# Optimization experiments

Hardware: AMD Instinct MI355X
Metric: run time of the kernel (lower is better)

## Reference

```python
import jax, jax.numpy as jnp
import numpy as np

N = 50000    # n_nodes
E = 800000   # n_edges (avg degree 16)
F_IN = 64    # node_features
F_H = 64     # filters


def setup_inputs() -> dict:
    key = jax.random.key(0)
    ks = jax.random.split(key, 24)
    p = lambda k, s: jax.random.normal(k, s, dtype=jnp.float32) * 0.05
    inp = {
        "x": jax.random.normal(ks[0], (N, F_IN), dtype=jnp.float32),
        "edge_index": jax.random.randint(ks[1], (2, E), 0, N, dtype=jnp.int32),
        "edge_weight": jax.random.uniform(ks[2], (E,), dtype=jnp.float32),
    }
    # 6 ChebConvs (K=2): conv_x_z, conv_h_z, conv_x_r, conv_h_r, conv_x_h, conv_h_h
    for i, nm in enumerate(["xz", "hz", "xr", "hr", "xh", "hh"]):
        fin = F_IN if nm[0] == "x" else F_H
        inp[f"W_{nm}0"] = p(ks[3 + 3 * i], (fin, F_H))
        inp[f"W_{nm}1"] = p(ks[4 + 3 * i], (fin, F_H))
        inp[f"b_{nm}"] = p(ks[5 + 3 * i], (F_H,))
    inp["W_lin"] = p(ks[21], (F_H, F_IN))
    inp["b_lin"] = p(ks[22], (F_IN,))
    return inp


def _forward(x, edge_weight, edge_index,
             W_xz0, W_xz1, b_xz, W_hz0, W_hz1, b_hz,
             W_xr0, W_xr1, b_xr, W_hr0, W_hr1, b_hr,
             W_xh0, W_xh1, b_xh, W_hh0, W_hh1, b_hh,
             W_lin, b_lin):
    row, col = edge_index[0], edge_index[1]
    # ChebConv K=2, sym normalization, lambda_max=2: L_hat = -D^{-1/2} A D^{-1/2}
    # (self-loops removed first, as in PyG ChebConv)
    w = jnp.where(row == col, 0.0, edge_weight)
    deg = jax.ops.segment_sum(w, row, num_segments=N)
    deg_safe = jnp.where(deg > 0, deg, 1.0)
    dinv = jnp.where(deg > 0, jax.lax.rsqrt(deg_safe), 0.0)
    norm = -dinv[row] * w * dinv[col]  # [E]

    def conv(v, W0, W1, b):
        # Tx_0 = v ; Tx_1 = L_hat @ v via gather-scatter along edges
        tx1 = jax.ops.segment_sum(norm[:, None] * v[row], col, num_segments=N)
        return v @ W0 + tx1 @ W1 + b

    H = jnp.zeros((N, F_H), dtype=x.dtype)  # initial hidden state
    Z = jax.nn.sigmoid(conv(x, W_xz0, W_xz1, b_xz) + conv(H, W_hz0, W_hz1, b_hz))
    R = jax.nn.sigmoid(conv(x, W_xr0, W_xr1, b_xr) + conv(H, W_hr0, W_hr1, b_hr))
    Ht = jnp.tanh(conv(x, W_xh0, W_xh1, b_xh) + conv(H * R, W_hh0, W_hh1, b_hh))
    H = Z * H + (1.0 - Z) * Ht
    return jax.nn.relu(H) @ W_lin + b_lin


def reference(x, edge_index, edge_weight,
              W_xz0, W_xz1, b_xz, W_hz0, W_hz1, b_hz,
              W_xr0, W_xr1, b_xr, W_hr0, W_hr1, b_hr,
              W_xh0, W_xh1, b_xh, W_hh0, W_hh1, b_hh,
              W_lin, b_lin):
    return _forward(x, edge_weight, edge_index,
                    W_xz0, W_xz1, b_xz, W_hz0, W_hz1, b_hz,
                    W_xr0, W_xr1, b_xr, W_hr0, W_hr1, b_hr,
                    W_xh0, W_xh1, b_xh, W_hh0, W_hh1, b_hh,
                    W_lin, b_lin)
```

## Files before the change

kernel.cpp:

```cpp
#include <hip/hip_runtime.h>

#define N_NODES 50000
#define N_EDGES 800000
#define F 64
#define NPAD 50048
#define NBUCK 196
#define NBLK 256
#define EPB (N_EDGES / NBLK)
#define BN 128
#define ASTRIDE 132

__global__ __launch_bounds__(256) void count_kernel(const int* __restrict__ ei,
                                                    int* __restrict__ cntC,
                                                    int* __restrict__ cntR) {
    __shared__ int histC[NBUCK], histR[NBUCK];
    const int t = threadIdx.x, blk = blockIdx.x;
    for (int i = t; i < NBUCK; i += 256) { histC[i] = 0; histR[i] = 0; }
    __syncthreads();
    const int e0 = blk * EPB;
    for (int i = t; i < EPB; i += 256) {
        int e = e0 + i;
        int r = ei[e], c = ei[N_EDGES + e];
        if (r != c) {
            atomicAdd(&histC[c >> 8], 1);
            atomicAdd(&histR[r >> 8], 1);
        }
    }
    __syncthreads();
    for (int i = t; i < NBUCK; i += 256) {
        cntC[i * NBLK + blk] = histC[i];
        cntR[i * NBLK + blk] = histR[i];
    }
}

__global__ __launch_bounds__(256) void scan1_kernel(int* __restrict__ cntC,
                                                    int* __restrict__ cntR,
                                                    int* __restrict__ btC,
                                                    int* __restrict__ btR) {
    __shared__ int wsum[4];
    const int t = threadIdx.x, g = blockIdx.x;
    int* cnt = (g < NBUCK) ? cntC : cntR;
    int* bt  = (g < NBUCK) ? btC : btR;
    const int bucket = (g < NBUCK) ? g : g - NBUCK;
    const int lane = t & 63, wid = t >> 6;
    int v = cnt[bucket * NBLK + t];
    int s = v;
#pragma unroll
    for (int d = 1; d < 64; d <<= 1) {
        int u = __shfl_up(s, d);
        if (lane >= d) s += u;
    }
    if (lane == 63) wsum[wid] = s;
    __syncthreads();
    int wbase = 0;
    for (int w = 0; w < wid; ++w) wbase += wsum[w];
    cnt[bucket * NBLK + t] = wbase + s - v;
    if (t == 255) bt[bucket] = wbase + s;
}

__global__ __launch_bounds__(256) void scan2_kernel(const int* __restrict__ btC,
                                                    const int* __restrict__ btR,
                                                    int* __restrict__ bbC,
                                                    int* __restrict__ bbR,
                                                    int* __restrict__ offs) {
    __shared__ int wsum[4];
    const int t = threadIdx.x;
    const int lane = t & 63, wid = t >> 6;
    {
        int v = (t < NBUCK) ? btC[t] : 0;
        int s = v;
#pragma unroll
        for (int d = 1; d < 64; d <<= 1) {
            int u = __shfl_up(s, d);
            if (lane >= d) s += u;
        }
        if (lane == 63) wsum[wid] = s;
        __syncthreads();
        int wbase = 0;
        for (int w = 0; w < wid; ++w) wbase += wsum[w];
        if (t < NBUCK) bbC[t] = wbase + s - v;
        if (t == 255) { bbC[NBUCK] = wbase + s; offs[N_NODES] = wbase + s; }
        __syncthreads();
    }
    {
        int v = (t < NBUCK) ? btR[t] : 0;
        int s = v;
#pragma unroll
        for (int d = 1; d < 64; d <<= 1) {
            int u = __shfl_up(s, d);
            if (lane >= d) s += u;
        }
        if (lane == 63) wsum[wid] = s;
        __syncthreads();
        int wbase = 0;
        for (int w = 0; w < wid; ++w) wbase += wsum[w];
        if (t < NBUCK) bbR[t] = wbase + s - v;
        if (t == 255) bbR[NBUCK] = wbase + s;
    }
}

__global__ __launch_bounds__(256) void place_kernel(const int* __restrict__ ei,
                                                    const float* __restrict__ ew,
                                                    const int* __restrict__ cntC,
                                                    const int* __restrict__ cntR,
                                                    const int* __restrict__ bbC,
                                                    const int* __restrict__ bbR,
                                                    uint2* __restrict__ colPart,
                                                    uint2* __restrict__ rowPart) {
    __shared__ int cursC[NBUCK], cursR[NBUCK];
    const int t = threadIdx.x, blk = blockIdx.x;
    for (int i = t; i < NBUCK; i += 256) {
        cursC[i] = bbC[i] + cntC[i * NBLK + blk];
        cursR[i] = bbR[i] + cntR[i * NBLK + blk];
    }
    __syncthreads();
    const int e0 = blk * EPB;
    for (int i = t; i < EPB; i += 256) {
        int e = e0 + i;
        int r = ei[e], c = ei[N_EDGES + e];
        if (r == c) continue;
        unsigned wbits = __float_as_uint(ew[e]);
        int pC = atomicAdd(&cursC[c >> 8], 1);
        colPart[pC] = make_uint2((unsigned)r | ((unsigned)(c & 255) << 16), wbits);
        int pR = atomicAdd(&cursR[r >> 8], 1);
        rowPart[pR] = make_uint2((unsigned)(r & 255), wbits);
    }
}

__global__ __launch_bounds__(256) void rowB_kernel(const uint2* __restrict__ rowPart,
                                                   const int* __restrict__ bbR,
                                                   float* __restrict__ dinv) {
    __shared__ float degL[256];
    const int t = threadIdx.x, b = blockIdx.x;
    degL[t] = 0.0f;
    __syncthreads();
    const int start = bbR[b], end = bbR[b + 1];
    for (int i = start + t; i < end; i += 256) {
        uint2 v = rowPart[i];
        atomicAdd(&degL[v.x], __uint_as_float(v.y));
    }
    __syncthreads();
    int n = b * 256 + t;
    if (n < N_NODES) {
        float d = degL[t];
        dinv[n] = (d > 0.0f) ? rsqrtf(d) : 0.0f;
    }
}

__global__ __launch_bounds__(256) void colB_kernel(const uint2* __restrict__ colPart,
                                                   const int* __restrict__ bbC,
                                                   const float* __restrict__ dinv,
                                                   int* __restrict__ offs,
                                                   uint2* __restrict__ edgesOut) {
    __shared__ int cntL[256];
    __shared__ int curL[256];
    __shared__ int wsum[4];
    const int t = threadIdx.x, b = blockIdx.x;
    const int lane = t & 63, wid = t >> 6;
    const int start = bbC[b], end = bbC[b + 1];
    cntL[t] = 0;
    __syncthreads();
    for (int i = start + t; i < end; i += 256) {
        uint2 v = colPart[i];
        atomicAdd(&cntL[(v.x >> 16) & 255], 1);
    }
    __syncthreads();
    int v = cntL[t];
    int s = v;
#pragma unroll
    for (int d = 1; d < 64; d <<= 1) {
        int u = __shfl_up(s, d);
        if (lane >= d) s += u;
    }
    if (lane == 63) wsum[wid] = s;
    __syncthreads();
    int wbase = 0;
    for (int w = 0; w < wid; ++w) wbase += wsum[w];
    int excl = wbase + s - v;
    curL[t] = excl;
    int n = b * 256 + t;
    if (n < N_NODES) offs[n] = start + excl;
    __syncthreads();
    for (int i = start + t; i < end; i += 256) {
        uint2 e = colPart[i];
        int cl = (e.x >> 16) & 255;
        int p = atomicAdd(&curL[cl], 1);
        int r = e.x & 0xFFFF;
        float wd = __uint_as_float(e.y) * dinv[r];
        edgesOut[start + p] = make_uint2((unsigned)r, __float_as_uint(wd));
    }
}

__global__ __launch_bounds__(256) void gather_kernel(const int* __restrict__ offs,
                                                     const uint2* __restrict__ edgesOut,
                                                     const float* __restrict__ dinv,
                                                     const float* __restrict__ x,
                                                     float* __restrict__ S) {
    int n = blockIdx.x * 4 + (threadIdx.x >> 6);
    int lane = threadIdx.x & 63;
    if (n >= N_NODES) return;
    int p = offs[n], end = offs[n + 1];
    float acc = 0.0f;
    for (int base = p; base < end; base += 32) {
        int rem = end - base;
        int sl = lane & 31;
        uint2 ev = make_uint2(0u, 0u);
        if (sl < rem) ev = edgesOut[base + sl];
        int myr = (int)ev.x;
        float mwd = __uint_as_float(ev.y);
        int cnt = min(rem, 32);
        int i = 0;
        for (; i + 4 <= cnt; i += 4) {
            int r0 = __shfl(myr, i + 0), r1 = __shfl(myr, i + 1);
            int r2 = __shfl(myr, i + 2), r3 = __shfl(myr, i + 3);
            float w0 = __shfl(mwd, i + 0), w1 = __shfl(mwd, i + 1);
            float w2 = __shfl(mwd, i + 2), w3 = __shfl(mwd, i + 3);
            float v0 = x[r0 * F + lane];
            float v1 = x[r1 * F + lane];
            float v2 = x[r2 * F + lane];
            float v3 = x[r3 * F + lane];
            acc = fmaf(w0, v0, acc);
            acc = fmaf(w1, v1, acc);
            acc = fmaf(w2, v2, acc);
            acc = fmaf(w3, v3, acc);
        }
        for (; i < cnt; ++i) {
            int r = __shfl(myr, i);
            float wd = __shfl(mwd, i);
            acc = fmaf(wd, x[r * F + lane], acc);
        }
    }
    S[n * F + lane] = -dinv[n] * acc;
}

__global__ __launch_bounds__(256) void fused_kernel(
    const float* __restrict__ x, float* sOut,
    const float* __restrict__ Wxz0, const float* __restrict__ Wxz1,
    const float* __restrict__ Wxh0, const float* __restrict__ Wxh1,
    const float* __restrict__ bxz, const float* __restrict__ bhz,
    const float* __restrict__ bxh, const float* __restrict__ bhh,
    const float* __restrict__ Wlin, const float* __restrict__ blin) {
    __shared__ float As[64 * ASTRIDE];
    __shared__ float Wc[32 * 128];

    const int t = threadIdx.x;
    const int n0 = blockIdx.x * BN;
    const int ti = t >> 4;
    const int tj = t & 15;
    const int f0 = tj * 4;

    float zacc[8][4], hacc[8][4];
#pragma unroll
    for (int j = 0; j < 4; ++j) {
        float bz = bxz[f0 + j] + bhz[f0 + j];
        float bh = bxh[f0 + j] + bhh[f0 + j];
#pragma unroll
        for (int i = 0; i < 8; ++i) { zacc[i][j] = bz; hacc[i][j] = bh; }
    }

    const int sn = t & 127;
    const int gn_s = n0 + sn;
    const int qb = t >> 7;

    for (int half = 0; half < 2; ++half) {
        const float* Abase = half ? (const float*)sOut : x;
#pragma unroll
        for (int r = 0; r < 8; ++r) {
            int q = r * 2 + qb;
            float4 v = make_float4(0.f, 0.f, 0.f, 0.f);
            if (gn_s < N_NODES) v = *(const float4*)&Abase[gn_s * F + q * 4];
            As[(q * 4 + 0) * ASTRIDE + sn] = v.x;
            As[(q * 4 + 1) * ASTRIDE + sn] = v.y;
            As[(q * 4 + 2) * ASTRIDE + sn] = v.z;
            As[(q * 4 + 3) * ASTRIDE + sn] = v.w;
        }
        const float* Wz = half ? Wxz1 : Wxz0;
        const float* Wh = half ? Wxh1 : Wxh0;
        for (int wchunk = 0; wchunk < 2; ++wchunk) {
            const int kb = wchunk * 32;
#pragma unroll
            for (int r = 0; r < 4; ++r) {
                int idx = r * 256 + t;
                int cq = idx & 31;
                int kk = idx >> 5;
                const float* src = (cq < 16) ? &Wz[(kb + kk) * F + cq * 4]
                                             : &Wh[(kb + kk) * F + (cq - 16) * 4];
                *(float4*)&Wc[kk * 128 + cq * 4] = *(const float4*)src;
            }
            __syncthreads();
#pragma unroll 8
            for (int kk = 0; kk < 32; ++kk) {
                const int kl = kb + kk;
                float4 a0 = *(const float4*)&As[kl * ASTRIDE + ti * 8];
                float4 a1 = *(const float4*)&As[kl * ASTRIDE + ti * 8 + 4];
                float4 wz = *(const float4*)&Wc[kk * 128 + f0];
                float4 wh = *(const float4*)&Wc[kk * 128 + 64 + f0];
                float a[8] = {a0.x, a0.y, a0.z, a0.w, a1.x, a1.y, a1.z, a1.w};
#pragma unroll
                for (int i = 0; i < 8; ++i) {
                    zacc[i][0] = fmaf(a[i], wz.x, zacc[i][0]);
                    zacc[i][1] = fmaf(a[i], wz.y, zacc[i][1]);
                    zacc[i][2] = fmaf(a[i], wz.z, zacc[i][2]);
                    zacc[i][3] = fmaf(a[i], wz.w, zacc[i][3]);
                    hacc[i][0] = fmaf(a[i], wh.x, hacc[i][0]);
                    hacc[i][1] = fmaf(a[i], wh.y, hacc[i][1]);
                    hacc[i][2] = fmaf(a[i], wh.z, hacc[i][2]);
                    hacc[i][3] = fmaf(a[i], wh.w, hacc[i][3]);
                }
            }
            __syncthreads();
        }
    }

#pragma unroll
    for (int j = 0; j < 4; ++j)
#pragma unroll
        for (int i = 0; i < 8; ++i) {
            float zz = 1.0f / (1.0f + __expf(-zacc[i][j]));
            float hh = tanhf(hacc[i][j]);
            float R = fmaxf((1.0f - zz) * hh, 0.0f);
            As[(f0 + j) * ASTRIDE + ti * 8 + i] = R;
        }
#pragma unroll
    for (int r = 0; r < 4; ++r) {
        int idx = r * 256 + t;
        int cq = idx & 15;
        int kk = idx >> 4;
        *(float4*)&Wc[kk * 64 + cq * 4] = *(const float4*)&Wlin[kk * F + cq * 4];
    }
    __syncthreads();

    float oacc[8][4];
#pragma unroll
    for (int j = 0; j < 4; ++j) {
        float bl = blin[f0 + j];
#pragma unroll
        for (int i = 0; i < 8; ++i) oacc[i][j] = bl;
    }
#pragma unroll 8
    for (int k = 0; k < 64; ++k) {
        float4 a0 = *(const float4*)&As[k * ASTRIDE + ti * 8];
        float4 a1 = *(const float4*)&As[k * ASTRIDE + ti * 8 + 4];
        float4 w = *(const float4*)&Wc[k * 64 + f0];
        float a[8] = {a0.x, a0.y, a0.z, a0.w, a1.x, a1.y, a1.z, a1.w};
#pragma unroll
        for (int i = 0; i < 8; ++i) {
            oacc[i][0] = fmaf(a[i], w.x, oacc[i][0]);
            oacc[i][1] = fmaf(a[i], w.y, oacc[i][1]);
            oacc[i][2] = fmaf(a[i], w.z, oacc[i][2]);
            oacc[i][3] = fmaf(a[i], w.w, oacc[i][3]);
        }
    }
#pragma unroll
    for (int i = 0; i < 8; ++i) {
        int gn = n0 + ti * 8 + i;
        if (gn < N_NODES) {
            float4 v = make_float4(oacc[i][0], oacc[i][1], oacc[i][2], oacc[i][3]);
            *(float4*)&sOut[gn * F + f0] = v;
        }
    }
}

__global__ __launch_bounds__(256) void deg_fb(const int* __restrict__ ei,
                                              const float* __restrict__ ew,
                                              float* __restrict__ deg) {
    int e = blockIdx.x * blockDim.x + threadIdx.x;
    if (e >= N_EDGES) return;
    int r = ei[e];
    int c = ei[N_EDGES + e];
    if (r != c) atomicAdd(&deg[r], ew[e]);
}

__global__ __launch_bounds__(256) void dinv_kernel(const float* __restrict__ deg,
                                                   float* __restrict__ dinv) {
    int n = blockIdx.x * blockDim.x + threadIdx.x;
    if (n >= N_NODES) return;
    float d = deg[n];
    dinv[n] = (d > 0.0f) ? rsqrtf(d) : 0.0f;
}

__global__ __launch_bounds__(256) void scatter_fb(const int* __restrict__ ei,
                                                  const float* __restrict__ ew,
                                                  const float* __restrict__ x,
                                                  const float* __restrict__ dinv,
                                                  float* S) {
    int e = blockIdx.x * 4 + (threadIdx.x >> 6);
    int lane = threadIdx.x & 63;
    if (e >= N_EDGES) return;
    int r = ei[e];
    int c = ei[N_EDGES + e];
    if (r == c) return;
    float nrm = -dinv[r] * ew[e] * dinv[c];
    atomicAdd(&S[c * F + lane], nrm * x[r * F + lane]);
}

extern "C" void kernel_launch(void* const* d_in, const int* in_sizes, int n_in,
                              void* d_out, int out_size, void* d_ws, size_t ws_size,
                              hipStream_t stream) {
    const float* x    = (const float*)d_in[0];
    const int*   ei   = (const int*)d_in[1];
    const float* ew   = (const float*)d_in[2];
    const float* Wxz0 = (const float*)d_in[3];
    const float* Wxz1 = (const float*)d_in[4];
    const float* bxz  = (const float*)d_in[5];
    const float* bhz  = (const float*)d_in[8];
    const float* Wxh0 = (const float*)d_in[15];
    const float* Wxh1 = (const float*)d_in[16];
    const float* bxh  = (const float*)d_in[17];
    const float* bhh  = (const float*)d_in[20];
    const float* Wlin = (const float*)d_in[21];
    const float* blin = (const float*)d_in[22];
    float* outp = (float*)d_out;

    int*    cntC  = (int*)d_ws;
    int*    cntR  = cntC + NBUCK * NBLK;
    int*    btC   = cntR + NBUCK * NBLK;
    int*    btR   = btC + 256;
    int*    bbC   = btR + 256;
    int*    bbR   = bbC + 256;
    int*    offs  = bbR + 256;
    float*  dinv  = (float*)(offs + NPAD + 64);
    uint2*  colPart  = (uint2*)(dinv + NPAD);
    uint2*  rowPart  = colPart + N_EDGES;
    uint2*  edgesOut = rowPart + N_EDGES;
    size_t needed = (size_t)(2 * NBUCK * NBLK + 1024 + NPAD + 64 + NPAD) * 4
                  + (size_t)N_EDGES * 3 * 8 + 256;

    if (ws_size >= needed) {
        count_kernel<<<NBLK, 256, 0, stream>>>(ei, cntC, cntR);
        scan1_kernel<<<2 * NBUCK, 256, 0, stream>>>(cntC, cntR, btC, btR);
        scan2_kernel<<<1, 256, 0, stream>>>(btC, btR, bbC, bbR, offs);
        place_kernel<<<NBLK, 256, 0, stream>>>(ei, ew, cntC, cntR, bbC, bbR,
                                               colPart, rowPart);
        rowB_kernel<<<NBUCK, 256, 0, stream>>>(rowPart, bbR, dinv);
        colB_kernel<<<NBUCK, 256, 0, stream>>>(colPart, bbC, dinv, offs, edgesOut);
        gather_kernel<<<(N_NODES + 3) / 4, 256, 0, stream>>>(offs, edgesOut, dinv,
                                                             x, outp);
    } else {
        float* deg = (float*)d_ws;
        float* dv  = deg + NPAD;
        hipMemsetAsync(deg, 0, (size_t)NPAD * sizeof(float), stream);
        hipMemsetAsync(d_out, 0, (size_t)N_NODES * F * sizeof(float), stream);
        deg_fb<<<(N_EDGES + 255) / 256, 256, 0, stream>>>(ei, ew, deg);
        dinv_kernel<<<(N_NODES + 255) / 256, 256, 0, stream>>>(deg, dv);
        scatter_fb<<<N_EDGES / 4, 256, 0, stream>>>(ei, ew, x, dv, outp);
    }
    fused_kernel<<<(N_NODES + BN - 1) / BN, 256, 0, stream>>>(
        x, outp, Wxz0, Wxz1, Wxh0, Wxh1, bxz, bhz, bxh, bhh, Wlin, blin);
}
```

Before: 123.3 us.

## Use 8x8 register tiles with 128 threads and padded LDS layout in fused GEMM

The fused GRU/linear kernel now uses 128 threads per block, with each thread computing an 8-node by 8-feature tile, where it previously computed 8x4. All 64 rows of each weight matrix are staged in LDS in a single pass, and the A tile gains extra padding every 8 rows to reduce bank conflicts. This raises FMA work per LDS load and removes barriers. In exchange it needs about twice the accumulator registers (128 floats) and more LDS, which may lower occupancy and leaves fewer threads per block to hide latency.

```diff
diff --git a/kernel.cpp b/kernel.cpp
--- a/kernel.cpp
+++ b/kernel.cpp
@@ -8,7 +8,7 @@
 #define NBLK 256
 #define EPB (N_EDGES / NBLK)
 #define BN 128
-#define ASTRIDE 132
+#define AIDX(k, n) ((k) * 132 + ((k) >> 3) * 4 + (n))
 
 __global__ __launch_bounds__(256) void count_kernel(const int* __restrict__ ei,
                                                     int* __restrict__ cntC,
@@ -233,130 +233,136 @@
     S[n * F + lane] = -dinv[n] * acc;
 }
 
-__global__ __launch_bounds__(256) void fused_kernel(
+__global__ __launch_bounds__(128) void fused_kernel(
     const float* __restrict__ x, float* sOut,
     const float* __restrict__ Wxz0, const float* __restrict__ Wxz1,
     const float* __restrict__ Wxh0, const float* __restrict__ Wxh1,
     const float* __restrict__ bxz, const float* __restrict__ bhz,
     const float* __restrict__ bxh, const float* __restrict__ bhh,
     const float* __restrict__ Wlin, const float* __restrict__ blin) {
-    __shared__ float As[64 * ASTRIDE];
-    __shared__ float Wc[32 * 128];
+    __shared__ float As[64 * 132 + 32];
+    __shared__ float Wc[64 * 128];
 
     const int t = threadIdx.x;
     const int n0 = blockIdx.x * BN;
-    const int ti = t >> 4;
-    const int tj = t & 15;
-    const int f0 = tj * 4;
-
-    float zacc[8][4], hacc[8][4];
-#pragma unroll
-    for (int j = 0; j < 4; ++j) {
+    const int ti = t >> 3;
+    const int tj = t & 7;
+    const int nb = ti * 8;
+    const int f0 = tj * 8;
+
+    float zacc[8][8], hacc[8][8];
+#pragma unroll
+    for (int j = 0; j < 8; ++j) {
         float bz = bxz[f0 + j] + bhz[f0 + j];
         float bh = bxh[f0 + j] + bhh[f0 + j];
 #pragma unroll
         for (int i = 0; i < 8; ++i) { zacc[i][j] = bz; hacc[i][j] = bh; }
     }
 
-    const int sn = t & 127;
-    const int gn_s = n0 + sn;
-    const int qb = t >> 7;
+    const int gn_s = n0 + t;
 
     for (int half = 0; half < 2; ++half) {
         const float* Abase = half ? (const float*)sOut : x;
 #pragma unroll
-        for (int r = 0; r < 8; ++r) {
-            int q = r * 2 + qb;
+        for (int q = 0; q < 16; ++q) {
             float4 v = make_float4(0.f, 0.f, 0.f, 0.f);
             if (gn_s < N_NODES) v = *(const float4*)&Abase[gn_s * F + q * 4];
-            As[(q * 4 + 0) * ASTRIDE + sn] = v.x;
-            As[(q * 4 + 1) * ASTRIDE + sn] = v.y;
-            As[(q * 4 + 2) * ASTRIDE + sn] = v.z;
-            As[(q * 4 + 3) * ASTRIDE + sn] = v.w;
+            As[AIDX(q * 4 + 0, t)] = v.x;
+            As[AIDX(q * 4 + 1, t)] = v.y;
+            As[AIDX(q * 4 + 2, t)] = v.z;
+            As[AIDX(q * 4 + 3, t)] = v.w;
         }
         const float* Wz = half ? Wxz1 : Wxz0;
         const float* Wh = half ? Wxh1 : Wxh0;
-        for (int wchunk = 0; wchunk < 2; ++wchunk) {
-            const int kb = wchunk * 32;
-#pragma unroll
-            for (int r = 0; r < 4; ++r) {
-                int idx = r * 256 + t;
-                int cq = idx & 31;
-                int kk = idx >> 5;
-                const float* src = (cq < 16) ? &Wz[(kb + kk) * F + cq * 4]
-                                             : &Wh[(kb + kk) * F + (cq - 16) * 4];
-                *(float4*)&Wc[kk * 128 + cq * 4] = *(const float4*)src;
-            }
-            __syncthreads();
+#pragma unroll
+        for (int r = 0; r < 16; ++r) {
+            int idx = r * 128 + t;
+            int cq = idx & 31;
+            int kk = idx >> 5;
+            const float* src = (cq < 16) ? &Wz[kk * F + cq * 4]
+                                         : &Wh[kk * F + (cq - 16) * 4];
+            *(float4*)&Wc[kk * 128 + cq * 4] = *(const float4*)src;
+        }
+        __syncthreads();
+
 #pragma unroll 8
-            for (int kk = 0; kk < 32; ++kk) {
-                const int kl = kb + kk;
-                float4 a0 = *(const float4*)&As[kl * ASTRIDE + ti * 8];
-                float4 a1 = *(const float4*)&As[kl * ASTRIDE + ti * 8 + 4];
-                float4 wz = *(const float4*)&Wc[kk * 128 + f0];
-                float4 wh = *(const float4*)&Wc[kk * 128 + 64 + f0];
-                float a[8] = {a0.x, a0.y, a0.z, a0.w, a1.x, a1.y, a1.z, a1.w};
-#pragma unroll
-                for (int i = 0; i < 8; ++i) {
-                    zacc[i][0] = fmaf(a[i], wz.x, zacc[i][0]);
-                    zacc[i][1] = fmaf(a[i], wz.y, zacc[i][1]);
-                    zacc[i][2] = fmaf(a[i], wz.z, zacc[i][2]);
-                    zacc[i][3] = fmaf(a[i], wz.w, zacc[i][3]);
-                    hacc[i][0] = fmaf(a[i], wh.x, hacc[i][0]);
-                    hacc[i][1] = fmaf(a[i], wh.y, hacc[i][1]);
-                    hacc[i][2] = fmaf(a[i], wh.z, hacc[i][2]);
-                    hacc[i][3] = fmaf(a[i], wh.w, hacc[i][3]);
+        for (int kl = 0; kl < 64; ++kl) {
+            const float* Ap = &As[AIDX(kl, nb)];
+            float4 a0 = *(const float4*)Ap;
+            float4 a1 = *(const float4*)(Ap + 4);
+            const float* Wp = &Wc[kl * 128 + f0];
+            float4 wz0 = *(const float4*)Wp;
+            float4 wz1 = *(const float4*)(Wp + 4);
+            float4 wh0 = *(const float4*)(Wp + 64);
+            float4 wh1 = *(const float4*)(Wp + 68);
+            float a[8]  = {a0.x, a0.y, a0.z, a0.w, a1.x, a1.y, a1.z, a1.w};
+            float wz[8] = {wz0.x, wz0.y, wz0.z, wz0.w, wz1.x, wz1.y, wz1.z, wz1.w};
+            float wh[8] = {wh0.x, wh0.y, wh0.z, wh0.w, wh1.x, wh1.y, wh1.z, wh1.w};
+#pragma unroll
+            for (int i = 0; i < 8; ++i)
+#pragma unroll
+                for (int j = 0; j < 8; ++j) {
+                    zacc[i][j] = fmaf(a[i], wz[j], zacc[i][j]);
+                    hacc[i][j] = fmaf(a[i], wh[j], hacc[i][j]);
                 }
-            }
-            __syncthreads();
-        }
-    }
-
-#pragma unroll
-    for (int j = 0; j < 4; ++j)
+        }
+        __syncthreads();
+    }
+
+#pragma unroll
+    for (int j = 0; j < 8; ++j) {
+        int f = f0 + j;
+        float R[8];
 #pragma unroll
         for (int i = 0; i < 8; ++i) {
             float zz = 1.0f / (1.0f + __expf(-zacc[i][j]));
             float hh = tanhf(hacc[i][j]);
-            float R = fmaxf((1.0f - zz) * hh, 0.0f);
-            As[(f0 + j) * ASTRIDE + ti * 8 + i] = R;
-        }
-#pragma unroll
-    for (int r = 0; r < 4; ++r) {
-        int idx = r * 256 + t;
+            R[i] = fmaxf((1.0f - zz) * hh, 0.0f);
+        }
+        float* Rp = &As[AIDX(f, nb)];
+        *(float4*)Rp = make_float4(R[0], R[1], R[2], R[3]);
+        *(float4*)(Rp + 4) = make_float4(R[4], R[5], R[6], R[7]);
+    }
+#pragma unroll
+    for (int r = 0; r < 8; ++r) {
+        int idx = r * 128 + t;
         int cq = idx & 15;
         int kk = idx >> 4;
         *(float4*)&Wc[kk * 64 + cq * 4] = *(const float4*)&Wlin[kk * F + cq * 4];
     }
     __syncthreads();
 
-    float oacc[8][4];
-#pragma unroll
-    for (int j = 0; j < 4; ++j) {
+    float (*oacc)[8] = zacc;
+#pragma unroll
+    for (int j = 0; j < 8; ++j) {
         float bl = blin[f0 + j];
 #pragma unroll
         for (int i = 0; i < 8; ++i) oacc[i][j] = bl;
     }
 #pragma unroll 8
     for (int k = 0; k < 64; ++k) {
-        float4 a0 = *(const float4*)&As[k * ASTRIDE + ti * 8];
-        float4 a1 = *(const float4*)&As[k * ASTRIDE + ti * 8 + 4];
-        float4 w = *(const float4*)&Wc[k * 64 + f0];
+        const float* Ap = &As[AIDX(k, nb)];
+        float4 a0 = *(const float4*)Ap;
+        float4 a1 = *(const float4*)(Ap + 4);
+        const float* Wp = &Wc[k * 64 + f0];
+        float4 w0 = *(const float4*)Wp;
+        float4 w1 = *(const float4*)(Wp + 4);
         float a[8] = {a0.x, a0.y, a0.z, a0.w, a1.x, a1.y, a1.z, a1.w};
-#pragma unroll
-        for (int i = 0; i < 8; ++i) {
-            oacc[i][0] = fmaf(a[i], w.x, oacc[i][0]);
-            oacc[i][1] = fmaf(a[i], w.y, oacc[i][1]);
-            oacc[i][2] = fmaf(a[i], w.z, oacc[i][2]);
-            oacc[i][3] = fmaf(a[i], w.w, oacc[i][3]);
-        }
+        float w[8] = {w0.x, w0.y, w0.z, w0.w, w1.x, w1.y, w1.z, w1.w};
+#pragma unroll
+        for (int i = 0; i < 8; ++i)
+#pragma unroll
+            for (int j = 0; j < 8; ++j)
+                oacc[i][j] = fmaf(a[i], w[j], oacc[i][j]);
     }
 #pragma unroll
     for (int i = 0; i < 8; ++i) {
-        int gn = n0 + ti * 8 + i;
+        int gn = n0 + nb + i;
         if (gn < N_NODES) {
-            float4 v = make_float4(oacc[i][0], oacc[i][1], oacc[i][2], oacc[i][3]);
-            *(float4*)&sOut[gn * F + f0] = v;
+            *(float4*)&sOut[gn * F + f0] =
+                make_float4(oacc[i][0], oacc[i][1], oacc[i][2], oacc[i][3]);
+            *(float4*)&sOut[gn * F + f0 + 4] =
+                make_float4(oacc[i][4], oacc[i][5], oacc[i][6], oacc[i][7]);
         }
     }
 }
@@ -445,6 +451,6 @@
         dinv_kernel<<<(N_NODES + 255) / 256, 256, 0, stream>>>(deg, dv);
         scatter_fb<<<N_EDGES / 4, 256, 0, stream>>>(ei, ew, x, dv, outp);
     }
-    fused_kernel<<<(N_NODES + BN - 1) / BN, 256, 0, stream>>>(
+    fused_kernel<<<(N_NODES + BN - 1) / BN, 128, 0, stream>>>(
         x, outp, Wxz0, Wxz1, Wxh0, Wxh1, bxz, bhz, bxh, bhh, Wlin, blin);
 }
```

Result: slower. 136.2 us (+10.5%).
